# Kernel optimization log

Measured on AMD Instinct MI355X. Metric: run time of the kernel, lower is better.

The kernel has to match this reference:

```python
import jax, jax.numpy as jnp
import numpy as np

B, T, U, L, C = 2048, 100, 512, 3, 10


def setup_inputs() -> dict:
    key = jax.random.key(0)
    ks = jax.random.split(key, 2 + 3 * L + 2)
    x = jax.random.normal(ks[0], (B, T, 1), dtype=jnp.float32)
    mask = jax.random.randint(ks[1], (B, T), 0, 2) > 0
    inp = {"x": x, "mask": mask}
    in_dim = 1
    s = 2
    for l in range(L):
        # Keras LSTM kernel layout: gates ordered [i, f, g(candidate), o]
        inp[f"W{l}"] = jax.random.normal(ks[s], (in_dim, 4 * U), dtype=jnp.float32) * 0.05
        inp[f"U{l}"] = jax.random.normal(ks[s + 1], (U, 4 * U), dtype=jnp.float32) * 0.05
        b = np.zeros((4 * U,), dtype=np.float32)
        b[U:2 * U] = 1.0  # unit_forget_bias (Keras default)
        inp[f"b{l}"] = jnp.asarray(b)
        in_dim = U
        s += 2
    inp["Wd"] = jax.random.normal(ks[s], (U, C), dtype=jnp.float32) * 0.05
    inp["bd"] = jnp.zeros((C,), dtype=jnp.float32)
    return inp


def _lstm_step(x_t, h, c, W, Uw, b):
    z = x_t @ W + h @ Uw + b  # [B, 4U]
    i, f, g, o = jnp.split(z, 4, axis=-1)
    i = jax.nn.sigmoid(i)
    f = jax.nn.sigmoid(f)
    g = jnp.tanh(g)
    o = jax.nn.sigmoid(o)
    c_new = f * c + i * g
    h_new = o * jnp.tanh(c_new)
    return h_new, c_new


def reference(x, mask, W0, U0, b0, W1, U1, b1, W2, U2, b2, Wd, bd):
    params = [(W0, U0, b0), (W1, U1, b1), (W2, U2, b2)]
    xt = jnp.swapaxes(x, 0, 1)        # [T, B, 1]
    mt = jnp.swapaxes(mask, 0, 1)     # [T, B]
    Bsz = x.shape[0]
    init = tuple((jnp.zeros((Bsz, U), x.dtype), jnp.zeros((Bsz, U), x.dtype)) for _ in range(L))

    def scan_fn(carry, inp_t):
        x_t, m_t = inp_t
        m = m_t[:, None]  # [B, 1]
        new_states = []
        layer_in = x_t
        for (h, c), (W, Uw, b) in zip(carry, params):
            h_new, c_new = _lstm_step(layer_in, h, c, W, Uw, b)
            # Keras mask semantics: masked steps carry state/output forward
            h_new = jnp.where(m, h_new, h)
            c_new = jnp.where(m, c_new, c)
            new_states.append((h_new, c_new))
            layer_in = h_new
        return tuple(new_states), None

    final, _ = jax.lax.scan(scan_fn, init, (xt, mt))
    h_top = final[-1][0]  # [B, U]
    logits = h_top @ Wd + bd
    return jax.nn.softmax(logits, axis=-1)
```

## Files before the change

### kernel.cpp

```cpp
#include <hip/hip_runtime.h>
#include <cstdint>
#include <cstddef>

#define B_   2048
#define T_   100
#define U_   512
#define NG_  2048
#define C_   10

typedef __attribute__((ext_vector_type(8))) short   short8;
typedef __attribute__((ext_vector_type(4))) float   floatx4;
typedef unsigned short ushort_t;

__device__ inline ushort_t f2bf(float f){
  unsigned u = __float_as_uint(f);
  unsigned r = (u + 0x7FFFu + ((u >> 16) & 1u)) >> 16;
  return (ushort_t)r;
}
__device__ inline float bf2f(ushort_t b){ return __uint_as_float(((unsigned)b) << 16); }

__device__ inline float sigm(float x){ return 1.0f / (1.0f + __expf(-x)); }
__device__ inline float tanh_fast(float x){
  float a = fabsf(x);
  float e = __expf(-2.0f * a);
  float r = (1.0f - e) / (1.0f + e);
  return copysignf(r, x);
}

__device__ inline int orig_col(int p){
  int Tt  = p >> 7;
  int loc = p & 127;
  int half = loc >> 6;
  int loc2 = loc & 63;
  int gate = loc2 >> 4;
  int uu   = (half << 4) | (loc2 & 15);
  return gate * U_ + Tt * 32 + uu;
}

#define AS1(p) ((const __attribute__((address_space(1))) void*)(p))
#define AS3(p) ((__attribute__((address_space(3))) void*)(p))

__global__ void convert_weights(
    const float* __restrict__ W0, const float* __restrict__ U0, const float* __restrict__ b0,
    const float* __restrict__ W1, const float* __restrict__ U1, const float* __restrict__ b1,
    const float* __restrict__ W2, const float* __restrict__ U2, const float* __restrict__ b2,
    ushort_t* __restrict__ Bt0, ushort_t* __restrict__ Bt1, ushort_t* __restrict__ Bt2,
    float* __restrict__ W0p, float* __restrict__ biasp)
{
  const int N0 = NG_ * 512;
  const int N1 = NG_ * 1024;
  const int total = N0 + 2 * N1 + NG_ + 3 * NG_;
  int idx = blockIdx.x * 256 + threadIdx.x;
  if (idx >= total) return;

  if (idx < N0){
    int p = idx >> 9, k = idx & 511;
    Bt0[idx] = f2bf(U0[(size_t)k * NG_ + orig_col(p)]);
  } else if (idx < N0 + N1){
    int j = idx - N0; int p = j >> 10, k = j & 1023;
    int oc = orig_col(p);
    float v = (k < 512) ? W1[(size_t)k * NG_ + oc] : U1[(size_t)(k - 512) * NG_ + oc];
    Bt1[j] = f2bf(v);
  } else if (idx < N0 + 2 * N1){
    int j = idx - N0 - N1; int p = j >> 10, k = j & 1023;
    int oc = orig_col(p);
    float v = (k < 512) ? W2[(size_t)k * NG_ + oc] : U2[(size_t)(k - 512) * NG_ + oc];
    Bt2[j] = f2bf(v);
  } else if (idx < N0 + 2 * N1 + NG_){
    int p = idx - N0 - 2 * N1;
    W0p[p] = W0[orig_col(p)];
  } else {
    int j = idx - N0 - 2 * N1 - NG_;
    int l = j >> 11, p = j & 2047;
    const float* bs = (l == 0) ? b0 : (l == 1) ? b1 : b2;
    biasp[j] = bs[orig_col(p)];
  }
}

template<int LAYER>
__device__ __forceinline__ void do_task(
    const ushort_t* __restrict__ A0,
    const ushort_t* __restrict__ A1,
    const ushort_t* __restrict__ Bt,
    const float* __restrict__ biasp,
    const float* __restrict__ W0p,
    const float* __restrict__ x,
    const int* __restrict__ mask,
    float* __restrict__ cbuf,
    const ushort_t* __restrict__ hprev,
    ushort_t* __restrict__ hout,
    int t, int mt, int nt,
    ushort_t* tA, ushort_t* tB)
{
  constexpr int NPHASE = (LAYER == 0) ? 1 : 2;
  constexpr bool IS_L0 = (LAYER == 0);
  constexpr int K = NPHASE * 512;

  const int tid  = threadIdx.x;
  const int wv   = tid >> 6;
  const int lane = tid & 63;
  const int qd   = lane >> 4;
  const int l16  = lane & 15;
  const int wave_m = wv >> 1;
  const int wave_n = wv & 1;
  const int m0 = mt * 128, n0 = nt * 128;

  floatx4 acc[4][4];
  #pragma unroll
  for (int i = 0; i < 4; ++i)
    #pragma unroll
    for (int j = 0; j < 4; ++j) acc[i][j] = (floatx4){0.f, 0.f, 0.f, 0.f};

  #pragma unroll
  for (int ph = 0; ph < NPHASE; ++ph){
    const ushort_t* A = (NPHASE == 2 && ph == 1) ? A1 : A0;
    for (int k0 = 0; k0 < 512; k0 += 32){
      #pragma unroll
      for (int cc2 = 0; cc2 < 2; ++cc2){
        int i  = cc2 * 256 + wv * 64 + lane;
        int r  = i >> 2, cc = i & 3;
        const ushort_t* ga = A + (size_t)(m0 + r) * U_ + k0 + cc * 8;
        __builtin_amdgcn_global_load_lds(AS1(ga), AS3(&tA[(cc2 * 256 + wv * 64) * 8]), 16, 0, 0);
        const ushort_t* gb = Bt + (size_t)(n0 + r) * K + ph * 512 + k0 + cc * 8;
        __builtin_amdgcn_global_load_lds(AS1(gb), AS3(&tB[(cc2 * 256 + wv * 64) * 8]), 16, 0, 0);
      }
      __syncthreads();

      short8 af[4], bfr[4];
      #pragma unroll
      for (int wm = 0; wm < 4; ++wm)
        af[wm] = *(const short8*)&tA[(wave_m * 64 + wm * 16 + l16) * 32 + qd * 8];
      #pragma unroll
      for (int wn = 0; wn < 4; ++wn)
        bfr[wn] = *(const short8*)&tB[(wave_n * 64 + wn * 16 + l16) * 32 + qd * 8];
      #pragma unroll
      for (int wm = 0; wm < 4; ++wm)
        #pragma unroll
        for (int wn = 0; wn < 4; ++wn)
          acc[wm][wn] = __builtin_amdgcn_mfma_f32_16x16x32_bf16(af[wm], bfr[wn], acc[wm][wn], 0, 0, 0);
      __syncthreads();
    }
  }

  const int u  = nt * 32 + wave_n * 16 + l16;
  const int pb = nt * 128 + wave_n * 64 + l16;
  const float bi = biasp[pb], bf_ = biasp[pb + 16], bg = biasp[pb + 32], bo = biasp[pb + 48];
  float wi = 0.f, wf = 0.f, wg = 0.f, wo = 0.f;
  if (IS_L0){ wi = W0p[pb]; wf = W0p[pb + 16]; wg = W0p[pb + 32]; wo = W0p[pb + 48]; }

  #pragma unroll
  for (int wm = 0; wm < 4; ++wm){
    #pragma unroll
    for (int reg = 0; reg < 4; ++reg){
      int b = m0 + wave_m * 64 + wm * 16 + qd * 4 + reg;
      float zi = acc[wm][0][reg] + bi;
      float zf = acc[wm][1][reg] + bf_;
      float zg = acc[wm][2][reg] + bg;
      float zo = acc[wm][3][reg] + bo;
      if (IS_L0){
        float xv = x[(size_t)b * T_ + t];
        zi += xv * wi; zf += xv * wf; zg += xv * wg; zo += xv * wo;
      }
      int mk = mask[(size_t)b * T_ + t];
      size_t su = (size_t)b * U_ + u;
      float c_old = cbuf[su];
      float i_ = sigm(zi), f_ = sigm(zf), g_ = tanh_fast(zg), o_ = sigm(zo);
      float c_new = f_ * c_old + i_ * g_;
      float h_new = o_ * tanh_fast(c_new);
      ushort_t hb = mk ? f2bf(h_new) : hprev[su];
      cbuf[su] = mk ? c_new : c_old;
      hout[su] = hb;
    }
  }
}

__global__ __launch_bounds__(256, 3) void lstm_phase(
    const ushort_t* __restrict__ Bt0, const ushort_t* __restrict__ Bt1,
    const ushort_t* __restrict__ Bt2, const float* __restrict__ biasp,
    const float* __restrict__ W0p, const float* __restrict__ x,
    const int* __restrict__ mask,
    ushort_t* h00, ushort_t* h01, ushort_t* h10, ushort_t* h11,
    ushort_t* h20, ushort_t* h21,
    float* c0, float* c1, float* c2,
    int s)
{
  __shared__ __align__(16) ushort_t tA[128 * 32];
  __shared__ __align__(16) ushort_t tB[128 * 32];

  const int lin  = blockIdx.x;
  const int task = lin % 3;
  const int tile = lin / 3;
  const int mt = tile >> 4, nt = tile & 15;

  ushort_t* h0[2] = {h00, h01};
  ushort_t* h1[2] = {h10, h11};
  ushort_t* h2[2] = {h20, h21};

  if (task == 0){
    if (s >= 100) return;
    int t = s, p = t & 1;
    do_task<0>(h0[p], nullptr, Bt0, biasp, W0p, x, mask,
               c0, h0[p], h0[p ^ 1], t, mt, nt, tA, tB);
  } else if (task == 1){
    if (s < 1 || s > 100) return;
    int t = s - 1, p = t & 1;
    do_task<1>(h0[p ^ 1], h1[p], Bt1, biasp + NG_, nullptr, x, mask,
               c1, h1[p], h1[p ^ 1], t, mt, nt, tA, tB);
  } else {
    if (s < 2) return;
    int t = s - 2, p = t & 1;
    do_task<2>(h1[p ^ 1], h2[p], Bt2, biasp + 2 * NG_, nullptr, x, mask,
               c2, h2[p], h2[p ^ 1], t, mt, nt, tA, tB);
  }
}

__global__ __launch_bounds__(256) void head_softmax(
    const ushort_t* __restrict__ h2, const float* __restrict__ Wd,
    const float* __restrict__ bd, float* __restrict__ out)
{
  int wv = threadIdx.x >> 6, lane = threadIdx.x & 63;
  int row = blockIdx.x * 4 + wv;
  const ushort_t* hr = h2 + (size_t)row * U_;

  float acc[C_];
  #pragma unroll
  for (int c = 0; c < C_; ++c) acc[c] = 0.f;

  short8 hv = *(const short8*)&hr[lane * 8];
  #pragma unroll
  for (int j = 0; j < 8; ++j){
    float hf = bf2f((ushort_t)hv[j]);
    int k = lane * 8 + j;
    #pragma unroll
    for (int c = 0; c < C_; ++c) acc[c] += hf * Wd[k * C_ + c];
  }
  #pragma unroll
  for (int c = 0; c < C_; ++c){
    float v = acc[c];
    #pragma unroll
    for (int off = 32; off > 0; off >>= 1) v += __shfl_xor(v, off);
    acc[c] = v + bd[c];
  }
  float mx = acc[0];
  #pragma unroll
  for (int c = 1; c < C_; ++c) mx = fmaxf(mx, acc[c]);
  float e[C_]; float s = 0.f;
  #pragma unroll
  for (int c = 0; c < C_; ++c){ e[c] = __expf(acc[c] - mx); s += e[c]; }
  float inv = 1.0f / s;
  if (lane == 0){
    #pragma unroll
    for (int c = 0; c < C_; ++c) out[(size_t)row * C_ + c] = e[c] * inv;
  }
}

extern "C" void kernel_launch(void* const* d_in, const int* in_sizes, int n_in,
                              void* d_out, int out_size, void* d_ws, size_t ws_size,
                              hipStream_t stream)
{
  const float* x  = (const float*)d_in[0];
  const int*  mask= (const int*)  d_in[1];
  const float* W0 = (const float*)d_in[2];
  const float* U0 = (const float*)d_in[3];
  const float* b0 = (const float*)d_in[4];
  const float* W1 = (const float*)d_in[5];
  const float* U1 = (const float*)d_in[6];
  const float* b1 = (const float*)d_in[7];
  const float* W2 = (const float*)d_in[8];
  const float* U2 = (const float*)d_in[9];
  const float* b2 = (const float*)d_in[10];
  const float* Wd = (const float*)d_in[11];
  const float* bd = (const float*)d_in[12];
  float* out = (float*)d_out;

  char* ws = (char*)d_ws;
  size_t off = 0;
  auto alloc = [&](size_t sz) -> char* {
    char* p = ws + off; off = (off + sz + 255) & ~(size_t)255; return p;
  };
  ushort_t* Bt0  = (ushort_t*)alloc((size_t)NG_ * 512 * 2);
  ushort_t* Bt1  = (ushort_t*)alloc((size_t)NG_ * 1024 * 2);
  ushort_t* Bt2  = (ushort_t*)alloc((size_t)NG_ * 1024 * 2);
  float*    W0p  = (float*)alloc((size_t)NG_ * 4);
  float*    biasp= (float*)alloc((size_t)3 * NG_ * 4);

  const size_t hsz = (size_t)B_ * U_ * 2;
  const size_t csz = (size_t)B_ * U_ * 4;
  char* state = alloc(6 * hsz + 3 * csz);
  ushort_t* hb[3][2]; float* cb[3];
  {
    char* pp = state;
    for (int l = 0; l < 3; ++l)
      for (int par = 0; par < 2; ++par){ hb[l][par] = (ushort_t*)pp; pp += hsz; }
    for (int l = 0; l < 3; ++l){ cb[l] = (float*)pp; pp += csz; }
  }

  hipMemsetAsync(state, 0, 6 * hsz + 3 * csz, stream);

  const int total = NG_ * 512 + 2 * NG_ * 1024 + NG_ + 3 * NG_;
  convert_weights<<<(total + 255) / 256, 256, 0, stream>>>(
      W0, U0, b0, W1, U1, b1, W2, U2, b2, Bt0, Bt1, Bt2, W0p, biasp);

  for (int s = 0; s < 102; ++s){
    lstm_phase<<<768, 256, 0, stream>>>(
        Bt0, Bt1, Bt2, biasp, W0p, x, mask,
        hb[0][0], hb[0][1], hb[1][0], hb[1][1], hb[2][0], hb[2][1],
        cb[0], cb[1], cb[2], s);
  }

  head_softmax<<<B_ / 4, 256, 0, stream>>>(hb[2][0], Wd, bd, out);
}
```

Before: 3.957 ms.

## Double K-tile depth to 64 with XOR-swizzled LDS layout and task-major block mapping

Each main-loop iteration now stages a K=64 slice instead of K=32, which halves the number of barrier pairs per GEMM and feeds two MFMA sub-steps per load. The LDS tiles are written with a rotated column swizzle, and the fragment reads use matching offsets to avoid bank conflicts. Block-to-task mapping changes from interleaved (lin%3) to contiguous groups of 256 blocks per layer task. The cost is doubled LDS per block (32KB), which may limit occupancy under the launch bound of 3 blocks.

```diff
diff --git a/kernel.cpp b/kernel.cpp
--- a/kernel.cpp
+++ b/kernel.cpp
@@ -105,6 +105,27 @@
   const int wave_n = wv & 1;
   const int m0 = mt * 128, n0 = nt * 128;
 
+  int srow[4], scol[4];
+  #pragma unroll
+  for (int cc2 = 0; cc2 < 4; ++cc2){
+    int i = cc2 * 256 + wv * 64 + lane;
+    srow[cc2] = i >> 3;
+    scol[cc2] = ((i & 7) + (i >> 3)) & 7;
+  }
+
+  int aoff[2][4], boff[2][4];
+  #pragma unroll
+  for (int ks = 0; ks < 2; ++ks){
+    #pragma unroll
+    for (int w = 0; w < 4; ++w){
+      int Ra = wave_m * 64 + w * 16 + l16;
+      int Rb = wave_n * 64 + w * 16 + l16;
+      int q  = ks * 4 + qd;
+      aoff[ks][w] = Ra * 64 + ((q - Ra) & 7) * 8;
+      boff[ks][w] = Rb * 64 + ((q - Rb) & 7) * 8;
+    }
+  }
+
   floatx4 acc[4][4];
   #pragma unroll
   for (int i = 0; i < 4; ++i)
@@ -114,30 +135,32 @@
   #pragma unroll
   for (int ph = 0; ph < NPHASE; ++ph){
     const ushort_t* A = (NPHASE == 2 && ph == 1) ? A1 : A0;
-    for (int k0 = 0; k0 < 512; k0 += 32){
+    for (int k0 = 0; k0 < 512; k0 += 64){
       #pragma unroll
-      for (int cc2 = 0; cc2 < 2; ++cc2){
-        int i  = cc2 * 256 + wv * 64 + lane;
-        int r  = i >> 2, cc = i & 3;
-        const ushort_t* ga = A + (size_t)(m0 + r) * U_ + k0 + cc * 8;
-        __builtin_amdgcn_global_load_lds(AS1(ga), AS3(&tA[(cc2 * 256 + wv * 64) * 8]), 16, 0, 0);
-        const ushort_t* gb = Bt + (size_t)(n0 + r) * K + ph * 512 + k0 + cc * 8;
-        __builtin_amdgcn_global_load_lds(AS1(gb), AS3(&tB[(cc2 * 256 + wv * 64) * 8]), 16, 0, 0);
+      for (int cc2 = 0; cc2 < 4; ++cc2){
+        int ibase = cc2 * 256 + wv * 64;
+        const ushort_t* ga = A + (size_t)(m0 + srow[cc2]) * U_ + k0 + scol[cc2] * 8;
+        __builtin_amdgcn_global_load_lds(AS1(ga), AS3(&tA[ibase * 8]), 16, 0, 0);
+        const ushort_t* gb = Bt + (size_t)(n0 + srow[cc2]) * K + ph * 512 + k0 + scol[cc2] * 8;
+        __builtin_amdgcn_global_load_lds(AS1(gb), AS3(&tB[ibase * 8]), 16, 0, 0);
       }
       __syncthreads();
 
-      short8 af[4], bfr[4];
       #pragma unroll
-      for (int wm = 0; wm < 4; ++wm)
-        af[wm] = *(const short8*)&tA[(wave_m * 64 + wm * 16 + l16) * 32 + qd * 8];
-      #pragma unroll
-      for (int wn = 0; wn < 4; ++wn)
-        bfr[wn] = *(const short8*)&tB[(wave_n * 64 + wn * 16 + l16) * 32 + qd * 8];
-      #pragma unroll
-      for (int wm = 0; wm < 4; ++wm)
+      for (int ks = 0; ks < 2; ++ks){
+        short8 af[4], bfr[4];
+        #pragma unroll
+        for (int wm = 0; wm < 4; ++wm)
+          af[wm] = *(const short8*)&tA[aoff[ks][wm]];
         #pragma unroll
         for (int wn = 0; wn < 4; ++wn)
-          acc[wm][wn] = __builtin_amdgcn_mfma_f32_16x16x32_bf16(af[wm], bfr[wn], acc[wm][wn], 0, 0, 0);
+          bfr[wn] = *(const short8*)&tB[boff[ks][wn]];
+        #pragma unroll
+        for (int wm = 0; wm < 4; ++wm)
+          #pragma unroll
+          for (int wn = 0; wn < 4; ++wn)
+            acc[wm][wn] = __builtin_amdgcn_mfma_f32_16x16x32_bf16(af[wm], bfr[wn], acc[wm][wn], 0, 0, 0);
+      }
       __syncthreads();
     }
   }
@@ -184,12 +207,12 @@
     float* c0, float* c1, float* c2,
     int s)
 {
-  __shared__ __align__(16) ushort_t tA[128 * 32];
-  __shared__ __align__(16) ushort_t tB[128 * 32];
+  __shared__ __align__(16) ushort_t tA[128 * 64];
+  __shared__ __align__(16) ushort_t tB[128 * 64];
 
   const int lin  = blockIdx.x;
-  const int task = lin % 3;
-  const int tile = lin / 3;
+  const int task = lin >> 8;
+  const int tile = lin & 255;
   const int mt = tile >> 4, nt = tile & 15;
 
   ushort_t* h0[2] = {h00, h01};
```

Result: faster. 3.480 ms (-12.0%).
